# Kernel optimization log

Measured on AMD Instinct MI355X. Metric: run time of the kernel, lower is better.

Reference implementation:

```python
import jax, jax.numpy as jnp
import numpy as np

IN_FEATURES = 4096
OUT_FEATURES = 4096
ALPHA = 0.008

def setup_inputs() -> dict:
    key = jax.random.key(0)
    k_x, k_w = jax.random.split(key)
    # int8-valued activations and weights, stored as their natural int/float forms
    x = jax.random.randint(k_x, (4, 2048, IN_FEATURES), -127, 128, dtype=jnp.int32)
    weight = jax.random.randint(k_w, (OUT_FEATURES, IN_FEATURES), -127, 128, dtype=jnp.int32).astype(jnp.float32)
    bias = jnp.zeros((1, OUT_FEATURES), dtype=jnp.float32)  # fp16 in module; fp32 here for math
    alpha = jnp.float32(ALPHA)
    return {"x": x, "weight": weight, "bias": bias, "alpha": alpha}

def reference(x, weight, bias, alpha):
    # x: [B, S, in], weight: [out, in] (int8 values cast to fp32), bias: [1, out]
    # In the original, rand_elements/mask_mul are zeros so hybrid path == plain path:
    #   y = F.linear(x.float(), weight.float()); fp_y = y*alpha + bias
    x_shape = x.shape
    xf = x.reshape(-1, x_shape[-1]).astype(jnp.float32)  # [N, in]
    y = jnp.einsum('ni,oi->no', xf, weight)              # fp32 GEMM, as in the module
    fp_y = y * alpha + bias
    out = jnp.clip(jnp.round(fp_y), -128, 127).astype(jnp.int8)
    return out.reshape(*x_shape[:-1], -1)
```

## Files before the change

### kernel.cpp

```cpp
#include <hip/hip_runtime.h>
#include <stdint.h>

typedef int int32x4  __attribute__((ext_vector_type(4)));
typedef int int32x16 __attribute__((ext_vector_type(16)));

#define IN_F   4096
#define OUT_F  4096
#define ROWS   8192

#define BM 256
#define BN 256
#define BK 64
#define NT (IN_F / BK)
#define TILE_LDS 32768
#define LDS_TOTAL (4 * TILE_LDS)

#define GLOAD_LDS16(g, l)                                                      \
  __builtin_amdgcn_global_load_lds(                                            \
      (const __attribute__((address_space(1))) void*)(g),                      \
      (__attribute__((address_space(3))) void*)(l), 16, 0, 0)

#define WAITV(n)                                                               \
  do {                                                                         \
    asm volatile("s_waitcnt vmcnt(" #n ")" ::: "memory");                      \
    __builtin_amdgcn_sched_barrier(0);                                         \
  } while (0)

__device__ __forceinline__ int pack4i(int a, int b, int c, int d) {
  return (a & 0xff) | ((b & 0xff) << 8) | ((c & 0xff) << 16) | (d << 24);
}

#define CVT_BLOCKS 2048
#define CVT_NX 8388608
#define CVT_NT 12582912
__global__ void __launch_bounds__(256) cvt_kernel(const int4* __restrict__ x,
                                                  const float4* __restrict__ w,
                                                  int* __restrict__ ox,
                                                  int* __restrict__ ow) {
  size_t i = (size_t)blockIdx.x * 256 + threadIdx.x;
  for (; i < CVT_NT; i += (size_t)CVT_BLOCKS * 256) {
    if (i < CVT_NX) {
      int4 a = x[i];
      ox[i] = pack4i(a.x, a.y, a.z, a.w);
    } else {
      size_t j = i - CVT_NX;
      float4 a = w[j];
      ow[j] = pack4i(__float2int_rn(a.x), __float2int_rn(a.y),
                     __float2int_rn(a.z), __float2int_rn(a.w));
    }
  }
}

__global__ void __launch_bounds__(512) gemm_i8_kernel(
    const int8_t* __restrict__ A8, const int8_t* __restrict__ B8,
    const float* __restrict__ bias, const float* __restrict__ alpha_p,
    int* __restrict__ out) {
  extern __shared__ int8_t lds[];

  const int t    = threadIdx.x;
  const int wave = t >> 6;
  const int lane = t & 63;
  const int l31  = lane & 31;
  const int hi   = lane >> 5;
  const int wm   = wave >> 2;
  const int wn   = wave & 3;

  const int flat = blockIdx.y * gridDim.x + blockIdx.x;
  const int wid  = (flat & 7) * 64 + (flat >> 3);
  const int bm   = wid >> 4;
  const int bn   = wid & 15;

  const int rS = t >> 2;
  const int cS = ((t & 3) ^ ((t >> 3) & 3)) * 16;
  const int8_t* ga = A8 + (size_t)(bm * BM + rS) * IN_F + cS;
  const int8_t* gb = B8 + (size_t)(bn * BN + rS) * IN_F + cS;
  const int ldst = t * 16;

  const int swz   = (l31 >> 1) & 3;
  const int arow0 = (wm * 128 + l31) * 4;
  const int brow0 = (wn * 64  + l31) * 4;

  int32x16 acc[4][2] = {};

  auto issue = [&](int tile) {
    int8_t* base = lds + (tile & 3) * TILE_LDS;
    const int k0 = tile * BK;
    GLOAD_LDS16(ga + k0,                      base + ldst);
    GLOAD_LDS16(ga + k0 + (size_t)128 * IN_F, base + 8192  + ldst);
    GLOAD_LDS16(gb + k0,                      base + 16384 + ldst);
    GLOAD_LDS16(gb + k0 + (size_t)128 * IN_F, base + 24576 + ldst);
  };

  auto compute = [&](int tile) {
    const int32x4* As4 = (const int32x4*)(lds + (tile & 3) * TILE_LDS);
    const int32x4* Bs4 = (const int32x4*)(lds + (tile & 3) * TILE_LDS + 16384);
#pragma unroll
    for (int ks = 0; ks < 2; ++ks) {
      const int ksw = (ks * 2 + hi) ^ swz;
      int32x4 af[4], bf[2];
#pragma unroll
      for (int i = 0; i < 4; ++i) af[i] = As4[arow0 + i * 128 + ksw];
#pragma unroll
      for (int i = 0; i < 2; ++i) bf[i] = Bs4[brow0 + i * 128 + ksw];
      __builtin_amdgcn_s_setprio(1);
#pragma unroll
      for (int mi = 0; mi < 4; ++mi)
#pragma unroll
        for (int ni = 0; ni < 2; ++ni)
          acc[mi][ni] = __builtin_amdgcn_mfma_i32_32x32x32_i8(
              af[mi], bf[ni], acc[mi][ni], 0, 0, 0);
      __builtin_amdgcn_s_setprio(0);
    }
  };

  issue(0); issue(1); issue(2);

  for (int tt = 0; tt < NT - 3; ++tt) {
    WAITV(8);
    __builtin_amdgcn_s_barrier();
    __builtin_amdgcn_sched_barrier(0);
    issue(tt + 3);
    compute(tt);
  }
  WAITV(8);
  __builtin_amdgcn_s_barrier();
  __builtin_amdgcn_sched_barrier(0);
  compute(NT - 3);
  WAITV(4);
  __builtin_amdgcn_s_barrier();
  __builtin_amdgcn_sched_barrier(0);
  compute(NT - 2);
  WAITV(0);
  __builtin_amdgcn_s_barrier();
  __builtin_amdgcn_sched_barrier(0);
  compute(NT - 1);

  const float alpha = *alpha_p;
#pragma unroll
  for (int mi = 0; mi < 4; ++mi) {
    const int rowt = bm * BM + wm * 128 + mi * 32 + hi * 4;
#pragma unroll
    for (int ni = 0; ni < 2; ++ni) {
      const int col = bn * BN + wn * 64 + ni * 32 + l31;
      const float bv = bias[col];
#pragma unroll
      for (int r = 0; r < 16; ++r) {
        const int row = rowt + (r & 3) + 8 * (r >> 2);
        float v = rintf((float)acc[mi][ni][r] * alpha + bv);
        v = fminf(fmaxf(v, -128.f), 127.f);
        out[(size_t)row * OUT_F + col] = (int)v;
      }
    }
  }
}

extern "C" void kernel_launch(void* const* d_in, const int* in_sizes, int n_in,
                              void* d_out, int out_size, void* d_ws, size_t ws_size,
                              hipStream_t stream) {
  const int*   x     = (const int*)d_in[0];
  const float* w     = (const float*)d_in[1];
  const float* bias  = (const float*)d_in[2];
  const float* alpha = (const float*)d_in[3];
  int* out = (int*)d_out;

  int8_t* x8 = (int8_t*)d_ws;
  int8_t* w8 = x8 + (size_t)ROWS * IN_F;

  static bool attr_done = false;
  if (!attr_done) {
    (void)hipFuncSetAttribute(reinterpret_cast<const void*>(gemm_i8_kernel),
                              hipFuncAttributeMaxDynamicSharedMemorySize,
                              LDS_TOTAL);
    attr_done = true;
  }

  cvt_kernel<<<CVT_BLOCKS, 256, 0, stream>>>((const int4*)x, (const float4*)w,
                                             (int*)x8, (int*)w8);

  dim3 grid(OUT_F / BN, ROWS / BM);
  gemm_i8_kernel<<<grid, 512, LDS_TOTAL, stream>>>(x8, w8, bias, alpha, out);
}
```

Measured before the change: 407.4 us.

## Use k-major LDS layout and split tile loads across two barrier-synchronized phases

```diff
diff --git a/kernel.cpp b/kernel.cpp
--- a/kernel.cpp
+++ b/kernel.cpp
@@ -20,9 +20,11 @@
       (const __attribute__((address_space(1))) void*)(g),                      \
       (__attribute__((address_space(3))) void*)(l), 16, 0, 0)
 
-#define WAITV(n)                                                               \
+#define GATE(N)                                                                \
   do {                                                                         \
-    asm volatile("s_waitcnt vmcnt(" #n ")" ::: "memory");                      \
+    asm volatile("s_waitcnt vmcnt(" #N ")" ::: "memory");                      \
+    __builtin_amdgcn_sched_barrier(0);                                         \
+    __builtin_amdgcn_s_barrier();                                              \
     __builtin_amdgcn_sched_barrier(0);                                         \
   } while (0)
 
@@ -70,70 +72,66 @@
   const int bm   = wid >> 4;
   const int bn   = wid & 15;
 
-  const int rS = t >> 2;
-  const int cS = ((t & 3) ^ ((t >> 3) & 3)) * 16;
-  const int8_t* ga = A8 + (size_t)(bm * BM + rS) * IN_F + cS;
-  const int8_t* gb = B8 + (size_t)(bn * BN + rS) * IN_F + cS;
+  const int rS = t & 255;
+  const int cS = (t >> 8) * 16;
+  const int8_t* gA = A8 + (size_t)(bm * BM + rS) * IN_F + cS;
+  const int8_t* gB = B8 + (size_t)(bn * BN + rS) * IN_F + cS;
   const int ldst = t * 16;
 
-  const int swz   = (l31 >> 1) & 3;
-  const int arow0 = (wm * 128 + l31) * 4;
-  const int brow0 = (wn * 64  + l31) * 4;
+  const int aoff = wm * 128 + l31;
+  const int boff = wn * 64  + l31;
 
   int32x16 acc[4][2] = {};
 
-  auto issue = [&](int tile) {
+  auto issueA = [&](int tile) {
     int8_t* base = lds + (tile & 3) * TILE_LDS;
     const int k0 = tile * BK;
-    GLOAD_LDS16(ga + k0,                      base + ldst);
-    GLOAD_LDS16(ga + k0 + (size_t)128 * IN_F, base + 8192  + ldst);
-    GLOAD_LDS16(gb + k0,                      base + 16384 + ldst);
-    GLOAD_LDS16(gb + k0 + (size_t)128 * IN_F, base + 24576 + ldst);
+    GLOAD_LDS16(gA + k0,      base + ldst);
+    GLOAD_LDS16(gA + k0 + 32, base + 8192 + ldst);
+  };
+  auto issueB = [&](int tile) {
+    int8_t* base = lds + (tile & 3) * TILE_LDS + 16384;
+    const int k0 = tile * BK;
+    GLOAD_LDS16(gB + k0,      base + ldst);
+    GLOAD_LDS16(gB + k0 + 32, base + 8192 + ldst);
   };
 
-  auto compute = [&](int tile) {
+  auto phase = [&](int tile, int ks, int itile, int mode) {
     const int32x4* As4 = (const int32x4*)(lds + (tile & 3) * TILE_LDS);
-    const int32x4* Bs4 = (const int32x4*)(lds + (tile & 3) * TILE_LDS + 16384);
+    const int32x4* Bs4 = As4 + 1024;
+    const int kb = (ks * 2 + hi) * 256;
+    int32x4 af[4], bf[2];
 #pragma unroll
-    for (int ks = 0; ks < 2; ++ks) {
-      const int ksw = (ks * 2 + hi) ^ swz;
-      int32x4 af[4], bf[2];
+    for (int mi = 0; mi < 4; ++mi) af[mi] = As4[kb + aoff + mi * 32];
 #pragma unroll
-      for (int i = 0; i < 4; ++i) af[i] = As4[arow0 + i * 128 + ksw];
+    for (int ni = 0; ni < 2; ++ni) bf[ni] = Bs4[kb + boff + ni * 32];
+    if (mode == 0) issueA(itile);
+    else if (mode == 1) issueB(itile);
+    __builtin_amdgcn_s_barrier();
+    asm volatile("s_waitcnt lgkmcnt(0)" ::: "memory");
+    __builtin_amdgcn_sched_barrier(0);
+    __builtin_amdgcn_s_setprio(1);
 #pragma unroll
-      for (int i = 0; i < 2; ++i) bf[i] = Bs4[brow0 + i * 128 + ksw];
-      __builtin_amdgcn_s_setprio(1);
+    for (int mi = 0; mi < 4; ++mi)
 #pragma unroll
-      for (int mi = 0; mi < 4; ++mi)
-#pragma unroll
-        for (int ni = 0; ni < 2; ++ni)
-          acc[mi][ni] = __builtin_amdgcn_mfma_i32_32x32x32_i8(
-              af[mi], bf[ni], acc[mi][ni], 0, 0, 0);
-      __builtin_amdgcn_s_setprio(0);
-    }
+      for (int ni = 0; ni < 2; ++ni)
+        acc[mi][ni] = __builtin_amdgcn_mfma_i32_32x32x32_i8(
+            af[mi], bf[ni], acc[mi][ni], 0, 0, 0);
+    __builtin_amdgcn_s_setprio(0);
   };
 
-  issue(0); issue(1); issue(2);
+  issueA(0); issueB(0);
+  issueA(1); issueB(1);
+  issueA(2); issueB(2);
 
   for (int tt = 0; tt < NT - 3; ++tt) {
-    WAITV(8);
-    __builtin_amdgcn_s_barrier();
-    __builtin_amdgcn_sched_barrier(0);
-    issue(tt + 3);
-    compute(tt);
+    GATE(8);
+    phase(tt, 0, tt + 3, 0);
+    phase(tt, 1, tt + 3, 1);
   }
-  WAITV(8);
-  __builtin_amdgcn_s_barrier();
-  __builtin_amdgcn_sched_barrier(0);
-  compute(NT - 3);
-  WAITV(4);
-  __builtin_amdgcn_s_barrier();
-  __builtin_amdgcn_sched_barrier(0);
-  compute(NT - 2);
-  WAITV(0);
-  __builtin_amdgcn_s_barrier();
-  __builtin_amdgcn_sched_barrier(0);
-  compute(NT - 1);
+  GATE(8); phase(NT - 3, 0, 0, 2); phase(NT - 3, 1, 0, 2);
+  GATE(4); phase(NT - 2, 0, 0, 2); phase(NT - 2, 1, 0, 2);
+  GATE(0); phase(NT - 1, 0, 0, 2); phase(NT - 1, 1, 0, 2);
 
   const float alpha = *alpha_p;
 #pragma unroll
```

New measurement: 451.3 us. 1.11x slower.
